# Performance work log

Measured on AMD Instinct MI355X. Metric: run time of the kernel, lower is better.

The kernel has to match this reference:

```python
import jax, jax.numpy as jnp
import numpy as np

IMAGE_W, IMAGE_H = 1024, 1024
STRIDES = [8, 16, 32, 64, 128]
TOP_N = 1000
MIN_SCORE = 0.05
NMS_THRESH = 0.6
MAX_DET = 100
NUM_CLASSES = 80
B = 16
SIZES = [(128, 128), (64, 64), (32, 32), (16, 16), (8, 8)]


def setup_inputs() -> dict:
    key = jax.random.key(0)
    ks = jax.random.split(key, 15)
    inp = {}
    i = 0
    for lvl, (H, W) in enumerate(SIZES):
        inp[f"cls_head_{lvl}"] = jax.random.normal(ks[i], (B, H, W, NUM_CLASSES), jnp.float32); i += 1
        inp[f"reg_head_{lvl}"] = jax.random.normal(ks[i], (B, H, W, 4), jnp.float32); i += 1
        inp[f"center_head_{lvl}"] = jax.random.normal(ks[i], (B, H, W, 1), jnp.float32); i += 1
    return inp


def _nms_single(scores, classes, boxes):
    # scores: [N] (invalid entries already set to -1), classes: [N] float, boxes: [N,4]
    areas = (boxes[:, 2] - boxes[:, 0]) * (boxes[:, 3] - boxes[:, 1])

    def body(i, st):
        sc, out_s, out_c, out_b = st
        j = jnp.argmax(sc)
        best = sc[j]
        valid = best > 0.0  # surviving scores are > MIN_SCORE > 0; suppressed/invalid are -1
        out_s = out_s.at[i].set(jnp.where(valid, best, -1.0))
        out_c = out_c.at[i].set(jnp.where(valid, classes[j], -1.0))
        out_b = out_b.at[i].set(jnp.where(valid, boxes[j], -jnp.ones((4,), boxes.dtype)))
        # IoU of chosen box vs all remaining candidates (greedy suppression)
        tl = jnp.maximum(boxes[:, :2], boxes[j, :2])
        br = jnp.minimum(boxes[:, 2:], boxes[j, 2:])
        wh = jnp.clip(br - tl, 0.0, None)
        inter = wh[:, 0] * wh[:, 1]
        union = jnp.clip(areas + areas[j] - inter, 0.0001, None)
        iou = inter / union
        sc = jnp.where(iou >= NMS_THRESH, -1.0, sc)
        sc = sc.at[j].set(-1.0)
        return (sc, out_s, out_c, out_b)

    init = (scores,
            -jnp.ones((MAX_DET,), scores.dtype),
            -jnp.ones((MAX_DET,), scores.dtype),
            -jnp.ones((MAX_DET, 4), boxes.dtype))
    _, out_s, out_c, out_b = jax.lax.fori_loop(0, MAX_DET, body, init)
    return out_s, out_c, out_b


def _decode(cls_heads, reg_heads, center_heads):
    scs, clss, regs, poss = [], [], [], []
    for c, r, ct, stride in zip(cls_heads, reg_heads, center_heads, STRIDES):
        Bh, H, W, _ = r.shape
        xs = (jnp.arange(W, dtype=jnp.float32) + 0.5) * stride
        ys = (jnp.arange(H, dtype=jnp.float32) + 0.5) * stride
        X, Y = jnp.meshgrid(xs, ys, indexing='xy')      # [H,W], X varies over w
        pos = jnp.stack([X, Y], -1).reshape(-1, 2)      # [HW,2] = (x_ctr, y_ctr)
        cls = jax.nn.sigmoid(c).reshape(Bh, -1, c.shape[-1])
        reg = jnp.exp(r).reshape(Bh, -1, 4)
        ctr = jax.nn.sigmoid(ct).reshape(Bh, -1)
        sc = jnp.sqrt(jnp.max(cls, axis=-1) * ctr)      # sqrt(cls_score * centerness)
        cl = jnp.argmax(cls, axis=-1)
        pos_b = jnp.broadcast_to(pos[None], (Bh,) + pos.shape)
        if sc.shape[1] >= TOP_N:
            sc, idx = jax.lax.top_k(sc, TOP_N)
            cl = jnp.take_along_axis(cl, idx, axis=1)
            reg = jnp.take_along_axis(reg, idx[..., None], axis=1)
            pos_b = jnp.take_along_axis(pos_b, idx[..., None], axis=1)
        scs.append(sc); clss.append(cl); regs.append(reg); poss.append(pos_b)
    sc = jnp.concatenate(scs, axis=1)                   # [B,N]
    cl = jnp.concatenate(clss, axis=1).astype(jnp.float32)
    reg = jnp.concatenate(regs, axis=1)                 # [B,N,4]
    pos = jnp.concatenate(poss, axis=1)                 # [B,N,2]
    # ltrb -> x1y1x2y2, truncate to int (torch .int()), clamp to image
    bb = jnp.concatenate([pos - reg[..., 0:2], pos + reg[..., 2:4]], axis=-1)
    bb = jnp.trunc(bb)
    bb = jnp.stack([jnp.clip(bb[..., 0], 0.0, None),
                    jnp.clip(bb[..., 1], 0.0, None),
                    jnp.clip(bb[..., 2], None, float(IMAGE_W - 1)),
                    jnp.clip(bb[..., 3], None, float(IMAGE_H - 1))], axis=-1)
    masked = jnp.where(sc > MIN_SCORE, sc, -1.0)
    return jax.vmap(_nms_single)(masked, cl, bb)


def reference(cls_head_0, reg_head_0, center_head_0,
              cls_head_1, reg_head_1, center_head_1,
              cls_head_2, reg_head_2, center_head_2,
              cls_head_3, reg_head_3, center_head_3,
              cls_head_4, reg_head_4, center_head_4):
    cls_heads = [cls_head_0, cls_head_1, cls_head_2, cls_head_3, cls_head_4]
    reg_heads = [reg_head_0, reg_head_1, reg_head_2, reg_head_3, reg_head_4]
    center_heads = [center_head_0, center_head_1, center_head_2, center_head_3, center_head_4]
    return _decode(cls_heads, reg_heads, center_heads)
```

## Files before the change

### kernel.cpp

```cpp
#include <hip/hip_runtime.h>
#include <math.h>

typedef unsigned int uint;
typedef unsigned long long u64;

constexpr int BATCH = 16;
constexpr int HW_TOTAL = 21824;
constexpr int NCAND = 3320;
constexpr int MAXDET = 100;

constexpr int FULL_KEY  = 0;
constexpr int FULL_CLS  = FULL_KEY + BATCH * HW_TOTAL;
constexpr int FULL_PBOX = FULL_CLS + BATCH * HW_TOTAL;
constexpr int CAND_KEY  = FULL_PBOX + BATCH * HW_TOTAL * 2;
constexpr int CAND_CLS  = CAND_KEY + BATCH * NCAND;
constexpr int CAND_PBOX = CAND_CLS + BATCH * NCAND;

struct Ptrs {
  const float* cls0; const float* reg0; const float* ctr0;
  const float* cls1; const float* reg1; const float* ctr1;
  const float* cls2; const float* reg2; const float* ctr2;
  const float* cls3; const float* reg3; const float* ctr3;
  const float* cls4; const float* reg4; const float* ctr4;
};

__device__ __forceinline__ float sigmoidf_(float x) { return 1.f / (1.f + expf(-x)); }

__device__ __forceinline__ uint pk_max16(uint a, uint b){ uint d; asm("v_pk_max_i16 %0, %1, %2" : "=v"(d) : "v"(a), "v"(b)); return d; }
__device__ __forceinline__ uint pk_min16(uint a, uint b){ uint d; asm("v_pk_min_i16 %0, %1, %2" : "=v"(d) : "v"(a), "v"(b)); return d; }
__device__ __forceinline__ uint pk_sub16(uint a, uint b){ uint d; asm("v_pk_sub_i16 %0, %1, %2" : "=v"(d) : "v"(a), "v"(b)); return d; }
__device__ __forceinline__ uint mul24(uint a, uint b){ uint d; asm("v_mul_u32_u24 %0, %1, %2" : "=v"(d) : "v"(a), "v"(b)); return d; }

__device__ __forceinline__ void scan4(float4 q, int kbase, float& M, float& M2, int& mi)
{
  float v; bool c;
  v = q.x; c = v > M; M2 = c ? M : fmaxf(M2, v); M = c ? v : M; mi = c ? kbase + 0 : mi;
  v = q.y; c = v > M; M2 = c ? M : fmaxf(M2, v); M = c ? v : M; mi = c ? kbase + 1 : mi;
  v = q.z; c = v > M; M2 = c ? M : fmaxf(M2, v); M = c ? v : M; mi = c ? kbase + 2 : mi;
  v = q.w; c = v > M; M2 = c ? M : fmaxf(M2, v); M = c ? v : M; mi = c ? kbase + 3 : mi;
}

__global__ __launch_bounds__(256) void decode_kernel(Ptrs p, uint* wsu)
{
  const int t = threadIdx.x;
  const int wv = t >> 6, lane = t & 63;
  const int g = lane >> 2, r = lane & 3;
  const int wpos0 = blockIdx.x * 64 + wv * 16;
  const int b = wpos0 / HW_TOTAL;
  const int hw0 = wpos0 - b * HW_TOTAL;

  const float *clsp, *regp, *ctrp;
  int lstart, lw, HWl; float stridef;
  if (hw0 < 16384)      { lstart = 0;     lw = 7; stridef = 8.f;   HWl = 16384; clsp = p.cls0; regp = p.reg0; ctrp = p.ctr0; }
  else if (hw0 < 20480) { lstart = 16384; lw = 6; stridef = 16.f;  HWl = 4096;  clsp = p.cls1; regp = p.reg1; ctrp = p.ctr1; }
  else if (hw0 < 21504) { lstart = 20480; lw = 5; stridef = 32.f;  HWl = 1024;  clsp = p.cls2; regp = p.reg2; ctrp = p.ctr2; }
  else if (hw0 < 21760) { lstart = 21504; lw = 4; stridef = 64.f;  HWl = 256;   clsp = p.cls3; regp = p.reg3; ctrp = p.ctr3; }
  else                  { lstart = 21760; lw = 3; stridef = 128.f; HWl = 64;    clsp = p.cls4; regp = p.reg4; ctrp = p.ctr4; }

  const long base = (long)b * HWl + (hw0 - lstart);
  const long row = base + g;
  const float4* c4 = reinterpret_cast<const float4*>(clsp) + row * 20;

  float4 buf[5];
  #pragma unroll
  for (int j = 0; j < 5; ++j) buf[j] = c4[r + 4 * j];

  float M = -INFINITY, M2 = -INFINITY; int mi = 0;
  #pragma unroll
  for (int j = 0; j < 5; ++j) scan4(buf[j], 4 * (r + 4 * j), M, M2, mi);

  #pragma unroll
  for (int ms_ = 1; ms_ <= 2; ms_ <<= 1) {
    float Mo  = __shfl_xor(M, ms_);
    float M2o = __shfl_xor(M2, ms_);
    int   mio = __shfl_xor(mi, ms_);
    float mn = fminf(M, Mo);
    M2 = fmaxf(mn, fmaxf(M2, M2o));
    bool take = (Mo > M) || (Mo == M && mio < mi);
    mi = take ? mio : mi;
    M  = fmaxf(M, Mo);
  }

  float sstar = sigmoidf_(M);
  float onem = 1.0f - sstar;
  float thr = (onem > 0.0f) ? (M - 8e-6f / onem) : INFINITY;
  float msig = sstar; int mfin = mi;
  if (!(M2 < thr)) {
    float ms = -1.f; int mj = 0;
    #pragma unroll
    for (int j = 0; j < 5; ++j) {
      float4 q = buf[j];
      int kb = 4 * (r + 4 * j);
      float s;
      s = sigmoidf_(q.x); if (s > ms) { ms = s; mj = kb + 0; }
      s = sigmoidf_(q.y); if (s > ms) { ms = s; mj = kb + 1; }
      s = sigmoidf_(q.z); if (s > ms) { ms = s; mj = kb + 2; }
      s = sigmoidf_(q.w); if (s > ms) { ms = s; mj = kb + 3; }
    }
    #pragma unroll
    for (int ms_ = 1; ms_ <= 2; ms_ <<= 1) {
      float mso = __shfl_xor(ms, ms_);
      int   mjo = __shfl_xor(mj, ms_);
      bool take = (mso > ms) || (mso == ms && mjo < mj);
      ms = take ? mso : ms;
      mj = take ? mjo : mj;
    }
    msig = ms; mfin = mj;
  }

  if (r == 0) {
    float4 r4 = reinterpret_cast<const float4*>(regp)[row];
    float ctr = ctrp[row];
    float scv = sqrtf(msig * sigmoidf_(ctr));

    int lhw = (hw0 - lstart) + g;
    int h = lhw >> lw, w = lhw - (h << lw);
    float x = ((float)w + 0.5f) * stridef;
    float y = ((float)h + 0.5f) * stridef;
    float x1 = fmaxf(truncf(x - expf(r4.x)), 0.f);
    float y1 = fmaxf(truncf(y - expf(r4.y)), 0.f);
    float x2 = fminf(truncf(x + expf(r4.z)), 1023.f);
    float y2 = fminf(truncf(y + expf(r4.w)), 1023.f);

    uint kraw = (scv > 0.05f) ? (__float_as_uint(scv) - 0x3D000000u) : 0u;
    uint ix1 = (uint)x1, iy1 = (uint)y1, ix2 = (uint)x2, iy2 = (uint)y2;
    uint2 pb = make_uint2(ix1 | (iy1 << 16), ix2 | (iy2 << 16));

    int idx = wpos0 + g;
    int hw = hw0 + g;
    float* wsf = (float*)wsu;
    wsu[FULL_KEY + idx] = kraw;
    wsf[FULL_CLS + idx] = (float)mfin;
    reinterpret_cast<uint2*>(wsu + FULL_PBOX)[idx] = pb;

    if (hw >= 21504) {
      int ci = b * NCAND + 3000 + (hw - 21504);
      wsu[CAND_KEY + ci] = kraw;
      wsf[CAND_CLS + ci] = (float)mfin;
      reinterpret_cast<uint2*>(wsu + CAND_PBOX)[ci] = pb;
    }
  }
}

template<int CH, int HW, int K>
__device__ void topk_impl(const uint* __restrict__ fsu, const float* __restrict__ fc,
                          const uint2* __restrict__ fpb,
                          uint* __restrict__ cs, float* __restrict__ cc,
                          uint2* __restrict__ cpb,
                          uint* stage, int* part)
{
  int t = threadIdx.x, lane = t & 63, wid = t >> 6;

  uint key[CH];
  constexpr int HALF = (HW > 8192) ? 8192 : HW;
  constexpr int ROUNDS = HW / HALF;
  #pragma unroll
  for (int rr = 0; rr < ROUNDS; ++rr) {
    int base = rr * HALF;
    for (int i = t; i < HALF; i += 1024)
      stage[i] = fsu[base + i];
    __syncthreads();
    int t0 = base / CH;
    if (t >= t0 && t < t0 + HALF / CH) {
      int off = t * CH - base;
      #pragma unroll
      for (int k = 0; k < CH; ++k) key[k] = stage[off + k];
    }
    __syncthreads();
  }

  uint lo = 0u, hi = 0x2800001u;
  while (hi - lo > 1u) {
    uint mid = (lo + hi) >> 1;
    int c = 0;
    #pragma unroll
    for (int k = 0; k < CH; ++k) c += (key[k] >= mid) ? 1 : 0;
    #pragma unroll
    for (int m = 1; m < 64; m <<= 1) c += __shfl_xor(c, m);
    if (lane == 0) part[wid] = c;
    __syncthreads();
    int tot = 0;
    #pragma unroll
    for (int w = 0; w < 16; ++w) tot += part[w];
    __syncthreads();
    if (tot >= K) lo = mid; else hi = mid;
  }

  int cgt = 0, ceq = 0;
  #pragma unroll
  for (int k = 0; k < CH; ++k) { cgt += (key[k] > lo) ? 1 : 0; ceq += (key[k] == lo) ? 1 : 0; }
  uint packed = ((uint)cgt << 16) | (uint)ceq;
  uint incl = packed;
  #pragma unroll
  for (int m = 1; m < 64; m <<= 1) {
    uint u = __shfl_up(incl, m);
    if (lane >= m) incl += u;
  }
  if (lane == 63) part[wid] = (int)incl;
  __syncthreads();
  uint wpre = 0, tot_all = 0;
  #pragma unroll
  for (int w = 0; w < 16; ++w) {
    uint pv = (uint)part[w];
    if (w < wid) wpre += pv;
    tot_all += pv;
  }
  uint excl = wpre + incl - packed;
  int rgt = (int)(excl >> 16);
  int req = (int)(tot_all >> 16) + (int)(excl & 0xFFFFu);

  #pragma unroll
  for (int k = 0; k < CH; ++k) {
    int i = t * CH + k;
    uint kk = key[k];
    int r = -1;
    if (kk > lo) r = rgt++;
    else if (kk == lo) r = req++;
    if (r >= 0 && r < K) {
      cs[r] = kk;
      cc[r] = fc[i];
      cpb[r] = fpb[i];
    }
  }
}

__global__ __launch_bounds__(1024) void topk_kernel(uint* wsu)
{
  __shared__ uint stage[8192];
  __shared__ int part[16];
  int b = blockIdx.x, lvl = blockIdx.y;
  int lstart, coff;
  if (lvl == 0)      { lstart = 0;     coff = 0;    }
  else if (lvl == 1) { lstart = 16384; coff = 1000; }
  else               { lstart = 20480; coff = 2000; }
  int fbase = b * HW_TOTAL + lstart;
  const uint* fsu = wsu + FULL_KEY + fbase;
  const float* fc = ((const float*)wsu) + FULL_CLS + fbase;
  const uint2* fpb = reinterpret_cast<const uint2*>(wsu + FULL_PBOX) + fbase;
  uint*  cs = wsu + CAND_KEY + b * NCAND + coff;
  float* cc = ((float*)wsu) + CAND_CLS + b * NCAND + coff;
  uint2* cpb = reinterpret_cast<uint2*>(wsu + CAND_PBOX) + b * NCAND + coff;

  if (lvl == 0)      topk_impl<16, 16384, 1000>(fsu, fc, fpb, cs, cc, cpb, stage, part);
  else if (lvl == 1) topk_impl<4,  4096,  1000>(fsu, fc, fpb, cs, cc, cpb, stage, part);
  else               topk_impl<1,  1024,  1000>(fsu, fc, fpb, cs, cc, cpb, stage, part);
}

__device__ __forceinline__ u64 shfl_xor_u64(u64 v, int m) {
  int lo = __shfl_xor((int)(uint)(v & 0xffffffffull), m);
  int hi = __shfl_xor((int)(uint)(v >> 32), m);
  return ((u64)(uint)hi << 32) | (u64)(uint)lo;
}
__device__ __forceinline__ u64 ce_shfl(u64 v, int j, bool up, int lane) {
  u64 p = shfl_xor_u64(v, j);
  bool keep_max = (((lane & j) == 0) == up);
  return keep_max ? (v > p ? v : p) : (v < p ? v : p);
}
__device__ __forceinline__ u64 ce_lds(u64 v, u64 p, uint i, uint j, uint k) {
  bool keep_max = (((i & j) == 0u) == ((i & k) == 0u));
  return keep_max ? (v > p ? v : p) : (v < p ? v : p);
}

__device__ __forceinline__ uint block_scan_excl(uint v, uint* partials, uint& total)
{
  int lane = threadIdx.x & 63, wv = threadIdx.x >> 6;
  uint incl = v;
  #pragma unroll
  for (int m = 1; m < 64; m <<= 1) {
    uint u = __shfl_up(incl, m);
    if (lane >= m) incl += u;
  }
  __syncthreads();
  if (lane == 63) partials[wv] = incl;
  __syncthreads();
  uint wpre = 0, tot = 0;
  #pragma unroll
  for (int w = 0; w < 16; ++w) {
    uint pv = partials[w];
    if (w < wv) wpre += pv;
    tot += pv;
  }
  total = tot;
  return wpre + incl - v;
}

__global__ __launch_bounds__(1024) void nms_kernel(const uint* __restrict__ wsu,
                                                   float* __restrict__ out)
{
  __shared__ uint hist[4096];
  __shared__ u64 items[1024];
  __shared__ uint2 boxo[3328];
  __shared__ uint partials[16];
  __shared__ int bsel_sh;

  const int b = blockIdx.x, t = threadIdx.x;
  const int lane = t & 63;
  const uint*  ck  = wsu + CAND_KEY + b * NCAND;
  const float* ccl = ((const float*)wsu) + CAND_CLS + b * NCAND;
  const uint2* cpb = reinterpret_cast<const uint2*>(wsu + CAND_PBOX) + b * NCAND;

  uint k0 = (t          < NCAND) ? ck[t]          : 0u;
  uint k1 = (t + 1024   < NCAND) ? ck[t + 1024]   : 0u;
  uint k2 = (t + 2048   < NCAND) ? ck[t + 2048]   : 0u;
  uint k3 = (t + 3072   < NCAND) ? ck[t + 3072]   : 0u;
  for (int i = t; i < 3328; i += 1024)
    boxo[i] = (i < NCAND) ? cpb[i] : make_uint2(0u, 0u);

  reinterpret_cast<uint4*>(hist)[t] = make_uint4(0u, 0u, 0u, 0u);
  if (t == 0) bsel_sh = 0;
  __syncthreads();

  if (k0) atomicAdd(&hist[k0 >> 14], 1u);
  if (k1) atomicAdd(&hist[k1 >> 14], 1u);
  if (k2) atomicAdd(&hist[k2 >> 14], 1u);
  if (k3) atomicAdd(&hist[k3 >> 14], 1u);
  __syncthreads();

  uint c[4]; uint s = 0;
  #pragma unroll
  for (int q = 0; q < 4; ++q) { c[q] = hist[4095 - (t * 4 + q)]; s += c[q]; }
  uint total;
  uint excl = block_scan_excl(s, partials, total);
  {
    uint cum = excl;
    #pragma unroll
    for (int q = 0; q < 4; ++q) {
      if (total >= 512u && cum < 512u && cum + c[q] >= 512u)
        bsel_sh = 4095 - (t * 4 + q);
      cum += c[q];
    }
  }
  __syncthreads();
  const uint B = (uint)bsel_sh;

  bool s0 = k0 && (k0 >> 14) >= B;
  bool s1 = k1 && (k1 >> 14) >= B;
  bool s2 = k2 && (k2 >> 14) >= B;
  bool s3 = k3 && (k3 >> 14) >= B;
  uint nsel = (uint)s0 + (uint)s1 + (uint)s2 + (uint)s3;
  items[t] = 0ull;
  uint tot2;
  uint pos = block_scan_excl(nsel, partials, tot2);
  if (s0) { if (pos < 1024u) items[pos] = ((u64)k0 << 32) | (u64)(0xFFFFu - (uint)t);          ++pos; }
  if (s1) { if (pos < 1024u) items[pos] = ((u64)k1 << 32) | (u64)(0xFFFFu - (uint)(t + 1024)); ++pos; }
  if (s2) { if (pos < 1024u) items[pos] = ((u64)k2 << 32) | (u64)(0xFFFFu - (uint)(t + 2048)); ++pos; }
  if (s3) { if (pos < 1024u) items[pos] = ((u64)k3 << 32) | (u64)(0xFFFFu - (uint)(t + 3072)); ++pos; }
  __syncthreads();

  u64 r = items[t];
  for (uint kk = 2; kk <= 1024; kk <<= 1) {
    for (uint j = kk >> 1; j > 0; j >>= 1) {
      if (j >= 64u) {
        items[t] = r;
        __syncthreads();
        u64 p = items[t ^ (int)j];
        r = ce_lds(r, p, (uint)t, j, kk);
        __syncthreads();
      } else {
        r = ce_shfl(r, (int)j, ((uint)t & kk) == 0u, lane);
      }
    }
  }
  items[t] = r;
  __syncthreads();

  if (t >= 64) return;

  uint sax = 0u, say = 0u, sa3a = 0u;
  uint sbx = 0u, sby = 0u, sa3b = 0u;
  uint rrank0 = 0xFFFFFFFFu, rrank1 = 0xFFFFFFFFu;
  int m = 0;
  bool done = false;

  for (int base = 0; base < 1024 && !done && m < MAXDET; base += 64) {
    u64 it = items[base + lane];
    uint mykey = (uint)(it >> 32);
    int myslot = 0xFFFF - (int)(it & 0xFFFFu);
    if (myslot > 3327) myslot = 0;
    uint2 mb = boxo[myslot];
    uint mwh = pk_sub16(mb.y, mb.x);
    uint mqa3 = 3u * mul24(mwh & 0xffffu, mwh >> 16);

    u64 deadmask = __ballot(mykey == 0u);
    int nv = deadmask ? (__ffsll((long long)deadmask) - 1) : 64;
    if (nv < 64) done = true;

    for (int s = 0; s < nv; ++s) {
      uint qx  = (uint)__builtin_amdgcn_readlane((int)mb.x, s);
      uint qy  = (uint)__builtin_amdgcn_readlane((int)mb.y, s);
      uint qa3 = (uint)__builtin_amdgcn_readlane((int)mqa3, s);

      uint tl = pk_max16(qx, sax), br = pk_min16(qy, say);
      uint wh = pk_max16(pk_sub16(br, tl), 0u);
      uint inter = mul24(wh & 0xffffu, wh >> 16);
      uint s3 = qa3 + sa3a; uint s3m = s3 > 1u ? s3 : 1u;
      bool sup0 = (lane < m) && ((inter << 3) >= s3m);

      tl = pk_max16(qx, sbx); br = pk_min16(qy, sby);
      wh = pk_max16(pk_sub16(br, tl), 0u);
      inter = mul24(wh & 0xffffu, wh >> 16);
      s3 = qa3 + sa3b; s3m = s3 > 1u ? s3 : 1u;
      bool sup1 = ((64 + lane) < m) && ((inter << 3) >= s3m);

      if (__ballot(sup0 || sup1) == 0ull) {
        int rank = base + s;
        if (m < 64) {
          if (lane == m)      { sax = qx; say = qy; sa3a = qa3; rrank0 = (uint)rank; }
        } else {
          if (lane == m - 64) { sbx = qx; sby = qy; sa3b = qa3; rrank1 = (uint)rank; }
        }
        ++m;
        if (m >= MAXDET) break;
      }
    }
  }

  float* outs = out;
  float* outc = out + BATCH * MAXDET;
  float4* outb = reinterpret_cast<float4*>(out + 2 * BATCH * MAXDET);
  {
    float s, cl; float4 bx;
    if (rrank0 != 0xFFFFFFFFu) {
      u64 it = items[rrank0];
      uint key = (uint)(it >> 32);
      int slot = 0xFFFF - (int)(it & 0xFFFFu);
      uint2 q = boxo[slot];
      s = __uint_as_float(key + 0x3D000000u);
      cl = ccl[slot];
      bx = make_float4((float)(q.x & 0xffffu), (float)(q.x >> 16),
                       (float)(q.y & 0xffffu), (float)(q.y >> 16));
    } else { s = -1.f; cl = -1.f; bx = make_float4(-1.f, -1.f, -1.f, -1.f); }
    outs[b * MAXDET + lane] = s;
    outc[b * MAXDET + lane] = cl;
    outb[b * MAXDET + lane] = bx;
  }
  if (lane < MAXDET - 64) {
    float s, cl; float4 bx;
    if (rrank1 != 0xFFFFFFFFu) {
      u64 it = items[rrank1];
      uint key = (uint)(it >> 32);
      int slot = 0xFFFF - (int)(it & 0xFFFFu);
      uint2 q = boxo[slot];
      s = __uint_as_float(key + 0x3D000000u);
      cl = ccl[slot];
      bx = make_float4((float)(q.x & 0xffffu), (float)(q.x >> 16),
                       (float)(q.y & 0xffffu), (float)(q.y >> 16));
    } else { s = -1.f; cl = -1.f; bx = make_float4(-1.f, -1.f, -1.f, -1.f); }
    outs[b * MAXDET + 64 + lane] = s;
    outc[b * MAXDET + 64 + lane] = cl;
    outb[b * MAXDET + 64 + lane] = bx;
  }
}

extern "C" void kernel_launch(void* const* d_in, const int* in_sizes, int n_in,
                              void* d_out, int out_size, void* d_ws, size_t ws_size,
                              hipStream_t stream)
{
  Ptrs p;
  p.cls0 = (const float*)d_in[0];  p.reg0 = (const float*)d_in[1];  p.ctr0 = (const float*)d_in[2];
  p.cls1 = (const float*)d_in[3];  p.reg1 = (const float*)d_in[4];  p.ctr1 = (const float*)d_in[5];
  p.cls2 = (const float*)d_in[6];  p.reg2 = (const float*)d_in[7];  p.ctr2 = (const float*)d_in[8];
  p.cls3 = (const float*)d_in[9];  p.reg3 = (const float*)d_in[10]; p.ctr3 = (const float*)d_in[11];
  p.cls4 = (const float*)d_in[12]; p.reg4 = (const float*)d_in[13]; p.ctr4 = (const float*)d_in[14];

  uint* wsu = (uint*)d_ws;
  float* out = (float*)d_out;

  decode_kernel<<<(4 * BATCH * HW_TOTAL) / 256, 256, 0, stream>>>(p, wsu);
  dim3 g2(BATCH, 3);
  topk_kernel<<<g2, 1024, 0, stream>>>(wsu);
  nms_kernel<<<BATCH, 1024, 0, stream>>>(wsu, out);
}
```

Before: 87.72 us.

## Replace bisection threshold search in top-k with two-pass radix histogram select

The top-k threshold was found by a ~26-step binary search, each step needing a block reduction and two barriers. It is replaced by a two-level radix select: a 13-bit shared-memory histogram on the high bits, a block scan to find the bucket holding the K-th key, then a second histogram on the low bits. This cuts the barrier count to a few, at the cost of shared-memory atomics, which may contend when keys cluster.

```diff
diff --git a/kernel.cpp b/kernel.cpp
--- a/kernel.cpp
+++ b/kernel.cpp
@@ -142,12 +142,35 @@
   }
 }
 
+__device__ __forceinline__ uint block_scan_excl(uint v, uint* partials, uint& total)
+{
+  int lane = threadIdx.x & 63, wv = threadIdx.x >> 6;
+  uint incl = v;
+  #pragma unroll
+  for (int m = 1; m < 64; m <<= 1) {
+    uint u = __shfl_up(incl, m);
+    if (lane >= m) incl += u;
+  }
+  __syncthreads();
+  if (lane == 63) partials[wv] = incl;
+  __syncthreads();
+  uint wpre = 0, tot = 0;
+  #pragma unroll
+  for (int w = 0; w < 16; ++w) {
+    uint pv = partials[w];
+    if (w < wv) wpre += pv;
+    tot += pv;
+  }
+  total = tot;
+  return wpre + incl - v;
+}
+
 template<int CH, int HW, int K>
 __device__ void topk_impl(const uint* __restrict__ fsu, const float* __restrict__ fc,
                           const uint2* __restrict__ fpb,
                           uint* __restrict__ cs, float* __restrict__ cc,
                           uint2* __restrict__ cpb,
-                          uint* stage, int* part)
+                          uint* scratch, uint* partials, int* part, uint* selsh)
 {
   int t = threadIdx.x, lane = t & 63, wid = t >> 6;
 
@@ -158,33 +181,57 @@
   for (int rr = 0; rr < ROUNDS; ++rr) {
     int base = rr * HALF;
     for (int i = t; i < HALF; i += 1024)
-      stage[i] = fsu[base + i];
+      scratch[i] = fsu[base + i];
     __syncthreads();
     int t0 = base / CH;
     if (t >= t0 && t < t0 + HALF / CH) {
       int off = t * CH - base;
       #pragma unroll
-      for (int k = 0; k < CH; ++k) key[k] = stage[off + k];
+      for (int k = 0; k < CH; ++k) key[k] = scratch[off + k];
     }
     __syncthreads();
   }
 
-  uint lo = 0u, hi = 0x2800001u;
-  while (hi - lo > 1u) {
-    uint mid = (lo + hi) >> 1;
-    int c = 0;
-    #pragma unroll
-    for (int k = 0; k < CH; ++k) c += (key[k] >= mid) ? 1 : 0;
-    #pragma unroll
-    for (int m = 1; m < 64; m <<= 1) c += __shfl_xor(c, m);
-    if (lane == 0) part[wid] = c;
-    __syncthreads();
-    int tot = 0;
-    #pragma unroll
-    for (int w = 0; w < 16; ++w) tot += part[w];
-    __syncthreads();
-    if (tot >= K) lo = mid; else hi = mid;
-  }
+  for (int i = t; i < 8192; i += 1024) scratch[i] = 0u;
+  __syncthreads();
+  #pragma unroll
+  for (int k = 0; k < CH; ++k) atomicAdd(&scratch[key[k] >> 13], 1u);
+  __syncthreads();
+  uint c8[8], s = 0;
+  #pragma unroll
+  for (int j = 0; j < 8; ++j) { c8[j] = scratch[8191 - (t * 8 + j)]; s += c8[j]; }
+  uint total;
+  uint cum = block_scan_excl(s, partials, total);
+  #pragma unroll
+  for (int j = 0; j < 8; ++j) {
+    if (cum < (uint)K && cum + c8[j] >= (uint)K) {
+      selsh[0] = (uint)(8191 - (t * 8 + j));
+      selsh[1] = cum;
+    }
+    cum += c8[j];
+  }
+  __syncthreads();
+  const uint T = selsh[0];
+  const uint Kp = (uint)K - selsh[1];
+
+  for (int i = t; i < 8192; i += 1024) scratch[i] = 0u;
+  __syncthreads();
+  #pragma unroll
+  for (int k = 0; k < CH; ++k)
+    if ((key[k] >> 13) == T) atomicAdd(&scratch[key[k] & 0x1FFFu], 1u);
+  __syncthreads();
+  uint d8[8], s2 = 0;
+  #pragma unroll
+  for (int j = 0; j < 8; ++j) { d8[j] = scratch[8191 - (t * 8 + j)]; s2 += d8[j]; }
+  uint tot2;
+  uint cum2 = block_scan_excl(s2, partials, tot2);
+  #pragma unroll
+  for (int j = 0; j < 8; ++j) {
+    if (cum2 < Kp && cum2 + d8[j] >= Kp) selsh[2] = (uint)(8191 - (t * 8 + j));
+    cum2 += d8[j];
+  }
+  __syncthreads();
+  const uint lo = (T << 13) | selsh[2];
 
   int cgt = 0, ceq = 0;
   #pragma unroll
@@ -196,6 +243,7 @@
     uint u = __shfl_up(incl, m);
     if (lane >= m) incl += u;
   }
+  __syncthreads();
   if (lane == 63) part[wid] = (int)incl;
   __syncthreads();
   uint wpre = 0, tot_all = 0;
@@ -226,8 +274,10 @@
 
 __global__ __launch_bounds__(1024) void topk_kernel(uint* wsu)
 {
-  __shared__ uint stage[8192];
+  __shared__ uint scratch[8192];
+  __shared__ uint partials[16];
   __shared__ int part[16];
+  __shared__ uint selsh[4];
   int b = blockIdx.x, lvl = blockIdx.y;
   int lstart, coff;
   if (lvl == 0)      { lstart = 0;     coff = 0;    }
@@ -241,9 +291,9 @@
   float* cc = ((float*)wsu) + CAND_CLS + b * NCAND + coff;
   uint2* cpb = reinterpret_cast<uint2*>(wsu + CAND_PBOX) + b * NCAND + coff;
 
-  if (lvl == 0)      topk_impl<16, 16384, 1000>(fsu, fc, fpb, cs, cc, cpb, stage, part);
-  else if (lvl == 1) topk_impl<4,  4096,  1000>(fsu, fc, fpb, cs, cc, cpb, stage, part);
-  else               topk_impl<1,  1024,  1000>(fsu, fc, fpb, cs, cc, cpb, stage, part);
+  if (lvl == 0)      topk_impl<16, 16384, 1000>(fsu, fc, fpb, cs, cc, cpb, scratch, partials, part, selsh);
+  else if (lvl == 1) topk_impl<4,  4096,  1000>(fsu, fc, fpb, cs, cc, cpb, scratch, partials, part, selsh);
+  else               topk_impl<1,  1024,  1000>(fsu, fc, fpb, cs, cc, cpb, scratch, partials, part, selsh);
 }
 
 __device__ __forceinline__ u64 shfl_xor_u64(u64 v, int m) {
@@ -259,29 +309,6 @@
 __device__ __forceinline__ u64 ce_lds(u64 v, u64 p, uint i, uint j, uint k) {
   bool keep_max = (((i & j) == 0u) == ((i & k) == 0u));
   return keep_max ? (v > p ? v : p) : (v < p ? v : p);
-}
-
-__device__ __forceinline__ uint block_scan_excl(uint v, uint* partials, uint& total)
-{
-  int lane = threadIdx.x & 63, wv = threadIdx.x >> 6;
-  uint incl = v;
-  #pragma unroll
-  for (int m = 1; m < 64; m <<= 1) {
-    uint u = __shfl_up(incl, m);
-    if (lane >= m) incl += u;
-  }
-  __syncthreads();
-  if (lane == 63) partials[wv] = incl;
-  __syncthreads();
-  uint wpre = 0, tot = 0;
-  #pragma unroll
-  for (int w = 0; w < 16; ++w) {
-    uint pv = partials[w];
-    if (w < wv) wpre += pv;
-    tot += pv;
-  }
-  total = tot;
-  return wpre + incl - v;
 }
 
 __global__ __launch_bounds__(1024) void nms_kernel(const uint* __restrict__ wsu,
```

After: 70.74 us. 19.4% less time.
